# Optimization experiments

Measured on AMD Instinct MI355X. Metric: run time of the kernel, lower is better.

The kernel has to match this reference:

```python
import math
import jax, jax.numpy as jnp
import numpy as np

B, CI, CO, K, WD, H = 8, 512, 512, 3, 512, 64


def setup_inputs() -> dict:
    key = jax.random.key(0)
    ks = jax.random.split(key, 8)
    x = jax.random.normal(ks[0], (B, CI, H, H), jnp.float32)
    style = jax.random.normal(ks[1], (B, WD), jnp.float32)
    noise = jax.random.normal(ks[2], (B, CO, H, H), jnp.float32)
    # learned params
    weight = jax.random.normal(ks[3], (1, CO, CI, K, K), jnp.float32)      # ModulatedConv2d.weight
    mod_weight = jax.random.normal(ks[4], (CI, WD), jnp.float32)            # EqualLinear.weight
    mod_bias = jnp.ones((CI,), jnp.float32)                                  # bias_init=1
    noise_weight = 0.1 * jnp.ones((1,), jnp.float32)                         # NoiseInjection.weight (nonzero for signal)
    act_bias = 0.01 * jax.random.normal(ks[5], (CO,), jnp.float32)           # FusedLeakyReLU.bias
    return {"x": x, "style": style, "noise": noise, "weight": weight,
            "mod_weight": mod_weight, "mod_bias": mod_bias,
            "noise_weight": noise_weight, "act_bias": act_bias}


def reference(x, style, noise, weight, mod_weight, mod_bias, noise_weight, act_bias):
    # EqualLinear modulation: scale = 1/sqrt(w_space_dim), lr_mul = 1
    eq_scale = 1.0 / math.sqrt(WD)
    s = style @ (mod_weight * eq_scale).T + mod_bias            # [B, CI]
    # modulate + demodulate per-sample weights
    conv_scale = 1.0 / math.sqrt(CI * K * K)                     # 1/sqrt(fan_in)
    w = conv_scale * weight * s[:, None, :, None, None]          # [B, CO, CI, K, K]
    demod = jax.lax.rsqrt(jnp.sum(w * w, axis=(2, 3, 4)) + 1e-8)  # [B, CO]
    w = w * demod[:, :, None, None, None]
    pad = K // 2

    def conv1(xi, wi):  # per-sample conv (equivalent to groups=batch trick)
        return jax.lax.conv_general_dilated(
            xi[None], wi, window_strides=(1, 1),
            padding=[(pad, pad), (pad, pad)],
            dimension_numbers=("NCHW", "OIHW", "NCHW"))[0]

    out = jax.vmap(conv1)(x, w)                                  # [B, CO, H, H]
    # noise injection (noise provided -> no normalization branch)
    out = out + noise_weight[0] * noise
    # fused leaky relu: leaky_relu(out + bias) * sqrt(2)
    out = jax.nn.leaky_relu(out + act_bias[None, :, None, None], 0.2) * math.sqrt(2.0)
    return out
```

## Files before the change

kernel.cpp:

```cpp
#include <hip/hip_runtime.h>
#include <hip/hip_bf16.h>

typedef unsigned short u16;
typedef short bf16x8 __attribute__((ext_vector_type(8)));
typedef float f32x4 __attribute__((ext_vector_type(4)));

#define EQ_SCALE   0.04419417382415922f
#define CONV_SCALE 0.014731391274719738f

#define WS_S   0
#define WS_ESC (16*1024)
#define WS_WSQ (32*1024)
#define WS_WT  (32*1024 + 1024*1024)
#define WS_XS  (WS_WT + 9*512*512*2)

__device__ __forceinline__ void gld16(void* l, const void* g) {
  __builtin_amdgcn_global_load_lds((const __attribute__((address_space(1))) void*)g,
                                   (__attribute__((address_space(3))) void*)l,
                                   16, 0, 0);
}

__device__ __forceinline__ u16 f2b_rne(float f) {
  union { float f; unsigned int i; } c; c.f = f;
  unsigned int r = (c.i + 0x7FFFu + ((c.i >> 16) & 1u)) >> 16;
  return (u16)r;
}

__global__ void k_style(const float* __restrict__ style, const float* __restrict__ mw,
                        const float* __restrict__ mb, float* __restrict__ s) {
  int idx = blockIdx.x * 256 + threadIdx.x;
  int b = idx >> 9, i = idx & 511;
  const float* sr = style + (b << 9);
  const float* wr = mw + (i << 9);
  float acc = 0.f;
  for (int j = 0; j < 512; ++j) acc += sr[j] * wr[j];
  s[idx] = acc * EQ_SCALE + mb[i];
}

__global__ void k_wsq(const float* __restrict__ w, float* __restrict__ wsq) {
  int idx = blockIdx.x * 256 + threadIdx.x;
  const float* p = w + idx * 9;
  float a = 0.f;
  for (int t = 0; t < 9; ++t) { float v = p[t]; a += v * v; }
  wsq[idx] = a;
}

__global__ void k_esc(const float* __restrict__ wsq, const float* __restrict__ s,
                      float* __restrict__ esc) {
  int idx = blockIdx.x * 256 + threadIdx.x;
  int b = idx >> 9, o = idx & 511;
  const float* wr = wsq + (o << 9);
  const float* sr = s + (b << 9);
  float a = 0.f;
  for (int i = 0; i < 512; ++i) { float sv = sr[i]; a += wr[i] * sv * sv; }
  esc[idx] = CONV_SCALE * rsqrtf(CONV_SCALE * CONV_SCALE * a + 1e-8f);
}

__global__ void k_wt(const float* __restrict__ w, u16* __restrict__ wt) {
  int idx = blockIdx.x * 256 + threadIdx.x;
  const float* p = w + idx * 9;
  for (int t = 0; t < 9; ++t) wt[t * 262144 + idx] = f2b_rne(p[t]);
}

__global__ void k_xs(const float* __restrict__ x, const float* __restrict__ s,
                     u16* __restrict__ xs) {
  __shared__ u16 tile[64 * 66];
  int by = blockIdx.x;
  int i0 = blockIdx.y << 6;
  int b = by >> 6, y = by & 63;
  int t = threadIdx.x, w = t >> 6, lane = t & 63;
  for (int k = 0; k < 16; ++k) {
    int il = w + (k << 2);
    int i = i0 + il;
    float v = x[((((b << 9) + i) << 6) | y) << 6 | lane] * s[(b << 9) + i];
    tile[lane * 66 + il] = f2b_rne(v);
  }
  __syncthreads();
  for (int k = 0; k < 16; ++k) {
    int xc = w + (k << 2);
    xs[((((b << 6) | y) << 6 | xc) << 9) + i0 + lane] = tile[xc * 66 + lane];
  }
}

__global__ void __launch_bounds__(512, 2) k_conv(
    const u16* __restrict__ wt, const u16* __restrict__ xs,
    const float* __restrict__ esc, const float* __restrict__ noise,
    const float* __restrict__ nwp, const float* __restrict__ abias,
    float* __restrict__ out) {
  __shared__ __align__(16) u16 ldsA[2][128 * 64];
  __shared__ __align__(16) u16 ldsB[2][384 * 64];

  const int t = threadIdx.x;
  const int w = t >> 6, lane = t & 63;
  const int wm = w >> 2, wn = w & 3;
  const int quad = lane >> 4, l15 = lane & 15;
  const int o0 = blockIdx.x << 7;
  const int nt = blockIdx.y;
  const int b = nt >> 4, y0 = (nt & 15) << 2;

  int bgOff[6];
#pragma unroll
  for (int j = 0; j < 6; ++j) {
    int c = j * 512 + t;
    int pos = c >> 3, swz = c & 7;
    int ci16 = swz ^ (pos & 7);
    int tr = pos >> 6, col = pos & 63;
    int yy = y0 - 1 + tr; yy = yy < 0 ? 0 : (yy > 63 ? 63 : yy);
    bgOff[j] = ((((b << 6) + yy) << 6) + col) * 512 + ci16 * 8;
  }
  int agOff[2];
#pragma unroll
  for (int j = 0; j < 2; ++j) {
    int c = j * 512 + t;
    int ol = c >> 3, swz = c & 7;
    int ci16 = swz ^ (ol & 7);
    agOff[j] = (o0 + ol) * 512 + ci16 * 8;
  }

  f32x4 acc[16];
#pragma unroll
  for (int i = 0; i < 16; ++i) acc[i] = (f32x4)0.f;

  int aBase[4], aXor[4];
#pragma unroll
  for (int mf = 0; mf < 4; ++mf) {
    int ol = wm * 64 + mf * 16 + l15;
    aBase[mf] = ol * 8;
    aXor[mf] = ol & 7;
  }

#pragma unroll
  for (int j = 0; j < 6; ++j)
    gld16(&ldsB[0][(j * 512 + w * 64) * 8], xs + bgOff[j]);
#pragma unroll
  for (int j = 0; j < 2; ++j)
    gld16(&ldsA[0][(j * 512 + w * 64) * 8], wt + agOff[j]);

#pragma unroll 1
  for (int cib = 0; cib < 8; ++cib) {
    const u16* bR = ldsB[cib & 1];
#pragma unroll
    for (int khw = 0; khw < 9; ++khw) {
      const int par = (cib + khw) & 1;
      __syncthreads();

      if (cib < 7 || khw < 8) {
        const int nkhw = (khw == 8) ? 0 : khw + 1;
        const int ncib = (khw == 8) ? cib + 1 : cib;
        u16* aW = (u16*)ldsA[par ^ 1];
#pragma unroll
        for (int j = 0; j < 2; ++j)
          gld16(aW + (j * 512 + w * 64) * 8,
                wt + agOff[j] + nkhw * 262144 + ncib * 64);
      }
      if (khw == 6 && cib < 7) {
        u16* bW = (u16*)ldsB[(cib & 1) ^ 1];
#pragma unroll
        for (int j = 0; j < 6; ++j)
          gld16(bW + (j * 512 + w * 64) * 8, xs + bgOff[j] + (cib + 1) * 64);
      }

      const u16* aR = ldsA[par];
      const int kh = khw / 3, kw = khw % 3;
      const int row_in = y0 + wn + kh - 1;
      if (row_in >= 0 && row_in < 64) {
        const int tr = wn + kh;
        int bBase[4], bXor[4];
        bool bz[4];
#pragma unroll
        for (int nf = 0; nf < 4; ++nf) {
          int colo = nf * 16 + l15;
          int ci = colo + kw - 1;
          bz[nf] = (ci < 0) | (ci > 63);
          ci &= 63;
          int pos = tr * 64 + ci;
          bBase[nf] = pos * 8;
          bXor[nf] = pos & 7;
        }
#pragma unroll
        for (int ks = 0; ks < 2; ++ks) {
          const int kci = ks * 4 + quad;
          bf16x8 af[4], bf[4];
#pragma unroll
          for (int mf = 0; mf < 4; ++mf)
            af[mf] = *(const bf16x8*)(aR + (aBase[mf] + (kci ^ aXor[mf])) * 8);
#pragma unroll
          for (int nf = 0; nf < 4; ++nf) {
            bf16x8 v = *(const bf16x8*)(bR + (bBase[nf] + (kci ^ bXor[nf])) * 8);
            bf16x8 z = {0, 0, 0, 0, 0, 0, 0, 0};
            bf[nf] = bz[nf] ? z : v;
          }
          __builtin_amdgcn_s_setprio(1);
#pragma unroll
          for (int mf = 0; mf < 4; ++mf)
#pragma unroll
            for (int nf = 0; nf < 4; ++nf)
              acc[mf * 4 + nf] = __builtin_amdgcn_mfma_f32_16x16x32_bf16(
                  af[mf], bf[nf], acc[mf * 4 + nf], 0, 0, 0);
          __builtin_amdgcn_s_setprio(0);
        }
      }
    }
  }

  const float nwv = nwp[0];
  const int y = y0 + wn;
#pragma unroll
  for (int mf = 0; mf < 4; ++mf) {
#pragma unroll
    for (int r = 0; r < 4; ++r) {
      int o = o0 + wm * 64 + mf * 16 + quad * 4 + r;
      float es = esc[(b << 9) + o];
      float ab = abias[o];
      int rowbase = ((((b << 9) + o) << 6) | y) << 6;
#pragma unroll
      for (int nf = 0; nf < 4; ++nf) {
        int col = nf * 16 + l15;
        int idx = rowbase | col;
        float v = acc[mf * 4 + nf][r] * es + nwv * noise[idx] + ab;
        v = (v < 0.f ? 0.2f * v : v) * 1.4142135623730951f;
        out[idx] = v;
      }
    }
  }
}

extern "C" void kernel_launch(void* const* d_in, const int* in_sizes, int n_in,
                              void* d_out, int out_size, void* d_ws, size_t ws_size,
                              hipStream_t stream) {
  const float* x      = (const float*)d_in[0];
  const float* style  = (const float*)d_in[1];
  const float* noise  = (const float*)d_in[2];
  const float* weight = (const float*)d_in[3];
  const float* mw     = (const float*)d_in[4];
  const float* mb     = (const float*)d_in[5];
  const float* nw     = (const float*)d_in[6];
  const float* ab     = (const float*)d_in[7];
  float* out = (float*)d_out;

  char* ws = (char*)d_ws;
  float* s   = (float*)(ws + WS_S);
  float* esc = (float*)(ws + WS_ESC);
  float* wsq = (float*)(ws + WS_WSQ);
  u16* wt    = (u16*)(ws + WS_WT);
  u16* xs    = (u16*)(ws + WS_XS);

  k_style<<<16, 256, 0, stream>>>(style, mw, mb, s);
  k_wsq<<<1024, 256, 0, stream>>>(weight, wsq);
  k_esc<<<16, 256, 0, stream>>>(wsq, s, esc);
  k_wt<<<1024, 256, 0, stream>>>(weight, wt);
  k_xs<<<dim3(512, 8), 256, 0, stream>>>(x, s, xs);
  k_conv<<<dim3(4, 128), 512, 0, stream>>>(wt, xs, esc, noise, nw, ab, out);
}
```

Before: 395.2 us.

## Wave-parallel style/demod reductions, zero-row buffer, XCD-aware block mapping, finer waitcnts

The style and demodulation kernels now assign one wavefront per output and reduce float4 loads with shuffles, replacing the serial 512-iteration per-thread loops that ran on only 16 blocks. Out-of-range input rows in the conv are handled by loading from a small zeroed buffer, so the per-row branch disappears and every wave always issues MFMAs. The conv block index is remapped so blocks sharing output channels land on the same XCD. Explicit s_waitcnt vmcnt and raw barriers let the B-tile prefetch stay in flight across one iteration. Launch bounds drop to one block per CU, and an extra zeroing kernel is launched each call.

```diff
diff --git a/kernel.cpp b/kernel.cpp
--- a/kernel.cpp
+++ b/kernel.cpp
@@ -2,6 +2,7 @@
 #include <hip/hip_bf16.h>
 
 typedef unsigned short u16;
+typedef unsigned long long u64;
 typedef short bf16x8 __attribute__((ext_vector_type(8)));
 typedef float f32x4 __attribute__((ext_vector_type(4)));
 
@@ -13,6 +14,7 @@
 #define WS_WSQ (32*1024)
 #define WS_WT  (32*1024 + 1024*1024)
 #define WS_XS  (WS_WT + 9*512*512*2)
+#define WS_Z   (WS_XS + 8*64*64*512*2)
 
 __device__ __forceinline__ void gld16(void* l, const void* g) {
   __builtin_amdgcn_global_load_lds((const __attribute__((address_space(1))) void*)g,
@@ -28,13 +30,21 @@
 
 __global__ void k_style(const float* __restrict__ style, const float* __restrict__ mw,
                         const float* __restrict__ mb, float* __restrict__ s) {
-  int idx = blockIdx.x * 256 + threadIdx.x;
-  int b = idx >> 9, i = idx & 511;
-  const float* sr = style + (b << 9);
-  const float* wr = mw + (i << 9);
+  int g = blockIdx.x * 4 + (threadIdx.x >> 6);
+  int lane = threadIdx.x & 63;
+  int b = g >> 9, i = g & 511;
+  const float4* sr = (const float4*)(style + (b << 9));
+  const float4* wr = (const float4*)(mw + (i << 9));
   float acc = 0.f;
-  for (int j = 0; j < 512; ++j) acc += sr[j] * wr[j];
-  s[idx] = acc * EQ_SCALE + mb[i];
+#pragma unroll
+  for (int j = 0; j < 2; ++j) {
+    float4 a = sr[lane * 2 + j];
+    float4 w4 = wr[lane * 2 + j];
+    acc += a.x * w4.x + a.y * w4.y + a.z * w4.z + a.w * w4.w;
+  }
+#pragma unroll
+  for (int off = 32; off; off >>= 1) acc += __shfl_xor(acc, off);
+  if (lane == 0) s[g] = acc * EQ_SCALE + mb[i];
 }
 
 __global__ void k_wsq(const float* __restrict__ w, float* __restrict__ wsq) {
@@ -47,13 +57,25 @@
 
 __global__ void k_esc(const float* __restrict__ wsq, const float* __restrict__ s,
                       float* __restrict__ esc) {
-  int idx = blockIdx.x * 256 + threadIdx.x;
-  int b = idx >> 9, o = idx & 511;
-  const float* wr = wsq + (o << 9);
-  const float* sr = s + (b << 9);
+  int g = blockIdx.x * 4 + (threadIdx.x >> 6);
+  int lane = threadIdx.x & 63;
+  int b = g >> 9, o = g & 511;
+  const float4* wr = (const float4*)(wsq + (o << 9));
+  const float4* sr = (const float4*)(s + (b << 9));
   float a = 0.f;
-  for (int i = 0; i < 512; ++i) { float sv = sr[i]; a += wr[i] * sv * sv; }
-  esc[idx] = CONV_SCALE * rsqrtf(CONV_SCALE * CONV_SCALE * a + 1e-8f);
+#pragma unroll
+  for (int j = 0; j < 2; ++j) {
+    float4 wv = wr[lane * 2 + j];
+    float4 sv = sr[lane * 2 + j];
+    a += wv.x * sv.x * sv.x + wv.y * sv.y * sv.y + wv.z * sv.z * sv.z + wv.w * sv.w * sv.w;
+  }
+#pragma unroll
+  for (int off = 32; off; off >>= 1) a += __shfl_xor(a, off);
+  if (lane == 0) esc[g] = CONV_SCALE * rsqrtf(CONV_SCALE * CONV_SCALE * a + 1e-8f);
+}
+
+__global__ void k_zero(u64* __restrict__ z) {
+  z[blockIdx.x * 256 + threadIdx.x] = 0ull;
 }
 
 __global__ void k_wt(const float* __restrict__ w, u16* __restrict__ wt) {
@@ -82,8 +104,9 @@
   }
 }
 
-__global__ void __launch_bounds__(512, 2) k_conv(
+__global__ void __launch_bounds__(512, 1) k_conv(
     const u16* __restrict__ wt, const u16* __restrict__ xs,
+    const u16* __restrict__ zbuf,
     const float* __restrict__ esc, const float* __restrict__ noise,
     const float* __restrict__ nwp, const float* __restrict__ abias,
     float* __restrict__ out) {
@@ -92,21 +115,27 @@
 
   const int t = threadIdx.x;
   const int w = t >> 6, lane = t & 63;
-  const int wm = w >> 2, wn = w & 3;
+  const int wm = w >> 2, wrw = w & 3;
   const int quad = lane >> 4, l15 = lane & 15;
-  const int o0 = blockIdx.x << 7;
-  const int nt = blockIdx.y;
+
+  const int flat = blockIdx.y * 4 + blockIdx.x;
+  const int xcd = flat & 7, rest = flat >> 3;
+  const int o0 = (xcd & 3) << 7;
+  const int nt = (rest << 1) | (xcd >> 2);
   const int b = nt >> 4, y0 = (nt & 15) << 2;
 
-  int bgOff[6];
+  const u16* bgp[6];
 #pragma unroll
   for (int j = 0; j < 6; ++j) {
     int c = j * 512 + t;
     int pos = c >> 3, swz = c & 7;
     int ci16 = swz ^ (pos & 7);
-    int tr = pos >> 6, col = pos & 63;
-    int yy = y0 - 1 + tr; yy = yy < 0 ? 0 : (yy > 63 ? 63 : yy);
-    bgOff[j] = ((((b << 6) + yy) << 6) + col) * 512 + ci16 * 8;
+    int col = pos & 63;
+    int yy = y0 - 1 + j;
+    if ((unsigned)yy < 64u)
+      bgp[j] = xs + ((((b << 6) + yy) << 6) + col) * 512 + ci16 * 8;
+    else
+      bgp[j] = zbuf + col * 512 + ci16 * 8;
   }
   int agOff[2];
 #pragma unroll
@@ -131,80 +160,83 @@
 
 #pragma unroll
   for (int j = 0; j < 6; ++j)
-    gld16(&ldsB[0][(j * 512 + w * 64) * 8], xs + bgOff[j]);
+    gld16(&ldsB[0][(j * 512 + w * 64) * 8], bgp[j]);
 #pragma unroll
   for (int j = 0; j < 2; ++j)
     gld16(&ldsA[0][(j * 512 + w * 64) * 8], wt + agOff[j]);
 
 #pragma unroll 1
   for (int cib = 0; cib < 8; ++cib) {
-    const u16* bR = ldsB[cib & 1];
+    const u16* bR = &ldsB[cib & 1][0];
 #pragma unroll
     for (int khw = 0; khw < 9; ++khw) {
+      if (khw == 7) { asm volatile("s_waitcnt vmcnt(6)" ::: "memory"); }
+      else         { asm volatile("s_waitcnt vmcnt(0)" ::: "memory"); }
+      __builtin_amdgcn_s_barrier();
+      __builtin_amdgcn_sched_barrier(0);
+
       const int par = (cib + khw) & 1;
-      __syncthreads();
-
-      if (cib < 7 || khw < 8) {
+      const u16* aR = &ldsA[par][0];
+
+      {
+        u16* aW = (u16*)&ldsA[par ^ 1][0];
         const int nkhw = (khw == 8) ? 0 : khw + 1;
-        const int ncib = (khw == 8) ? cib + 1 : cib;
-        u16* aW = (u16*)ldsA[par ^ 1];
+        const int ncib = (khw == 8) ? ((cib + 1) & 7) : cib;
 #pragma unroll
         for (int j = 0; j < 2; ++j)
           gld16(aW + (j * 512 + w * 64) * 8,
                 wt + agOff[j] + nkhw * 262144 + ncib * 64);
       }
-      if (khw == 6 && cib < 7) {
-        u16* bW = (u16*)ldsB[(cib & 1) ^ 1];
+      if (khw == 6) {
+        u16* bW = (u16*)&ldsB[(cib & 1) ^ 1][0];
+        const int pc = (cib + 1) & 7;
 #pragma unroll
         for (int j = 0; j < 6; ++j)
-          gld16(bW + (j * 512 + w * 64) * 8, xs + bgOff[j] + (cib + 1) * 64);
-      }
-
-      const u16* aR = ldsA[par];
+          gld16(bW + (j * 512 + w * 64) * 8, bgp[j] + pc * 64);
+      }
+
       const int kh = khw / 3, kw = khw % 3;
-      const int row_in = y0 + wn + kh - 1;
-      if (row_in >= 0 && row_in < 64) {
-        const int tr = wn + kh;
-        int bBase[4], bXor[4];
-        bool bz[4];
+      const int tr = wrw + kh;
+      int bBase[4], bXor[4];
+      unsigned cmask[4];
+#pragma unroll
+      for (int nf = 0; nf < 4; ++nf) {
+        int ci = nf * 16 + l15 + kw - 1;
+        cmask[nf] = ((kw == 0 && nf == 0) || (kw == 2 && nf == 3))
+                        ? (unsigned)((unsigned)ci > 63u) : 0u;
+        ci &= 63;
+        int pos = tr * 64 + ci;
+        bBase[nf] = pos * 8;
+        bXor[nf] = pos & 7;
+      }
+#pragma unroll
+      for (int ks = 0; ks < 2; ++ks) {
+        const int kci = ks * 4 + quad;
+        bf16x8 af[4], bv[4];
+#pragma unroll
+        for (int mf = 0; mf < 4; ++mf)
+          af[mf] = *(const bf16x8*)(aR + (aBase[mf] + (kci ^ aXor[mf])) * 8);
 #pragma unroll
         for (int nf = 0; nf < 4; ++nf) {
-          int colo = nf * 16 + l15;
-          int ci = colo + kw - 1;
-          bz[nf] = (ci < 0) | (ci > 63);
-          ci &= 63;
-          int pos = tr * 64 + ci;
-          bBase[nf] = pos * 8;
-          bXor[nf] = pos & 7;
+          bf16x8 v = *(const bf16x8*)(bR + (bBase[nf] + (kci ^ bXor[nf])) * 8);
+          bf16x8 z = {0, 0, 0, 0, 0, 0, 0, 0};
+          bv[nf] = cmask[nf] ? z : v;
         }
-#pragma unroll
-        for (int ks = 0; ks < 2; ++ks) {
-          const int kci = ks * 4 + quad;
-          bf16x8 af[4], bf[4];
-#pragma unroll
-          for (int mf = 0; mf < 4; ++mf)
-            af[mf] = *(const bf16x8*)(aR + (aBase[mf] + (kci ^ aXor[mf])) * 8);
-#pragma unroll
-          for (int nf = 0; nf < 4; ++nf) {
-            bf16x8 v = *(const bf16x8*)(bR + (bBase[nf] + (kci ^ bXor[nf])) * 8);
-            bf16x8 z = {0, 0, 0, 0, 0, 0, 0, 0};
-            bf[nf] = bz[nf] ? z : v;
-          }
-          __builtin_amdgcn_s_setprio(1);
-#pragma unroll
-          for (int mf = 0; mf < 4; ++mf)
-#pragma unroll
-            for (int nf = 0; nf < 4; ++nf)
-              acc[mf * 4 + nf] = __builtin_amdgcn_mfma_f32_16x16x32_bf16(
-                  af[mf], bf[nf], acc[mf * 4 + nf], 0, 0, 0);
-          __builtin_amdgcn_s_setprio(0);
-        }
+        __builtin_amdgcn_s_setprio(1);
+#pragma unroll
+        for (int mf = 0; mf < 4; ++mf)
+#pragma unroll
+          for (int nf = 0; nf < 4; ++nf)
+            acc[mf * 4 + nf] = __builtin_amdgcn_mfma_f32_16x16x32_bf16(
+                af[mf], bv[nf], acc[mf * 4 + nf], 0, 0, 0);
+        __builtin_amdgcn_s_setprio(0);
       }
     }
   }
+  asm volatile("s_waitcnt vmcnt(0)" ::: "memory");
 
   const float nwv = nwp[0];
-  const int y = y0 + wn;
+  const int y = y0 + wrw;
 #pragma unroll
   for (int mf = 0; mf < 4; ++mf) {
 #pragma unroll
@@ -244,11 +276,13 @@
   float* wsq = (float*)(ws + WS_WSQ);
   u16* wt    = (u16*)(ws + WS_WT);
   u16* xs    = (u16*)(ws + WS_XS);
-
-  k_style<<<16, 256, 0, stream>>>(style, mw, mb, s);
+  u16* zbuf  = (u16*)(ws + WS_Z);
+
+  k_zero<<<32, 256, 0, stream>>>((u64*)zbuf);
+  k_style<<<1024, 256, 0, stream>>>(style, mw, mb, s);
   k_wsq<<<1024, 256, 0, stream>>>(weight, wsq);
-  k_esc<<<16, 256, 0, stream>>>(wsq, s, esc);
+  k_esc<<<1024, 256, 0, stream>>>(wsq, s, esc);
   k_wt<<<1024, 256, 0, stream>>>(weight, wt);
   k_xs<<<dim3(512, 8), 256, 0, stream>>>(x, s, xs);
-  k_conv<<<dim3(4, 128), 512, 0, stream>>>(wt, xs, esc, noise, nw, ab, out);
-}
+  k_conv<<<dim3(4, 128), 512, 0, stream>>>(wt, xs, zbuf, esc, noise, nw, ab, out);
+}
```

Result: faster. 365.0 us (-7.6%).
